# Kernel tuning notes

Hardware: AMD Instinct MI355X
Metric: run time of the kernel (lower is better)

The kernel has to match this reference:

```python
import jax, jax.numpy as jnp
import numpy as np

S0 = 192
C = [16, 32, 48, 64, 80]      # nPlanes = m*i, m=16, 5 strides
SL = [192, 96, 48, 24, 12]    # spatial size per level
OFF27 = jnp.asarray(np.stack(np.meshgrid(*([[-1, 0, 1]] * 3), indexing='ij'), -1).reshape(-1, 3), jnp.int32)
OFF8 = jnp.asarray(np.stack(np.meshgrid(*([[0, 1]] * 3), indexing='ij'), -1).reshape(-1, 3), jnp.int32)


def _flat(c, S):
    return (c[..., 0] * S + c[..., 1]) * S + c[..., 2]


def _grid(coords, S):
    g = jnp.full((S * S * S,), -1, jnp.int32)
    return g.at[_flat(coords, S)].set(jnp.arange(coords.shape[0], dtype=jnp.int32))


def _subconv(feat, coords, grid, S, W):
    # submanifold 3x3x3 conv over active sites only; W: [27, a, b]
    nb = coords[:, None, :] + OFF27                      # [N,27,3]
    valid = jnp.all((nb >= 0) & (nb < S), axis=-1)
    idx = grid[_flat(jnp.clip(nb, 0, S - 1), S)]         # [N,27]
    valid = valid & (idx >= 0)
    g = jnp.where(valid[..., None], feat[jnp.maximum(idx, 0)], 0.0)
    return jnp.einsum('nka,kab->nb', g, W)


def _downconv(feat, grid_f, S_f, out_coords, W):
    # kernel-2 stride-2 sparse conv; W: [8, a, b]
    src = out_coords[:, None, :] * 2 + OFF8              # [M,8,3]
    valid = jnp.all(src < S_f, axis=-1)
    idx = grid_f[_flat(src, S_f)]
    valid = valid & (idx >= 0)
    g = jnp.where(valid[..., None], feat[jnp.maximum(idx, 0)], 0.0)
    return jnp.einsum('nka,kab->nb', g, W)


def _bnrelu(x, g, b, eps=1e-4):
    # BatchNormLeakyReLU(leakiness=0) == BN (batch stats over active sites) + ReLU
    mu = jnp.mean(x, 0)
    var = jnp.mean((x - mu) ** 2, 0)
    return jax.nn.relu((x - mu) * jax.lax.rsqrt(var + eps) * g + b)


def _unpool(feat_c, grid_c, S_c, fine_coords, k):
    # UnPooling x k levels: copy coarse parent feature to each fine active site
    return feat_c[grid_c[_flat(fine_coords // (1 << k), S_c)]]


def _selection(scores):
    return (jax.nn.softmax(scores, axis=1)[:, 1:2] > 0.5).astype(scores.dtype)


def _forward(coords, features, w_in, blk_w, blk_g, blk_b, dn_g, dn_b, dn_w,
             ppn1_w, ppn1_sw, ppn2_w, ppn2_sw, ppn3_w, ppn3_pw, ppn3_sw):
    grids = [_grid(coords[l], SL[l]) for l in range(5)]
    x = _subconv(features, coords[0], grids[0], SL[0], w_in)   # input layer
    fmaps = [x]
    for i in range(4):  # encoder levels with residual blocks + downsample
        for r in range(2):
            h = _bnrelu(x, blk_g[i][2 * r], blk_b[i][2 * r])
            h = _subconv(h, coords[i], grids[i], SL[i], blk_w[i][2 * r])
            h = _bnrelu(h, blk_g[i][2 * r + 1], blk_b[i][2 * r + 1])
            h = _subconv(h, coords[i], grids[i], SL[i], blk_w[i][2 * r + 1])
            x = x + h  # ConcatTable(Identity, conv path) + AddTable, a==b
        x = _downconv(_bnrelu(x, dn_g[i], dn_b[i]), grids[i], SL[i], coords[i + 1], dn_w[i])
        fmaps.append(x)
    x = _subconv(x, coords[4], grids[4], SL[4], ppn1_w)
    ppn1_scores = x @ ppn1_sw                                   # 1x1 conv
    att1 = _unpool(_selection(ppn1_scores), grids[4], SL[4], coords[2], 2)
    y = fmaps[2] * att1                                         # Multiply at half_stride
    y = _subconv(y, coords[2], grids[2], SL[2], ppn2_w)
    ppn2_scores = y @ ppn2_sw
    att2 = _unpool(_selection(ppn2_scores), grids[2], SL[2], coords[0], 2)
    z = fmaps[0] * att2
    z = _subconv(z, coords[0], grids[0], SL[0], ppn3_w)
    out0 = jnp.concatenate([z @ ppn3_pw, z @ ppn3_sw], axis=1)
    out1 = jnp.concatenate([coords[4].astype(out0.dtype), ppn1_scores], axis=1)
    out2 = jnp.concatenate([coords[2].astype(out0.dtype), ppn2_scores], axis=1)
    return out0, out1, out2


def _make_coords():
    rng = np.random.RandomState(0)
    c0 = np.unique(rng.randint(0, S0, size=(100000, 3)), axis=0).astype(np.int32)
    cs = [c0]
    for _ in range(4):
        cs.append(np.unique(cs[-1] // 2, axis=0).astype(np.int32))
    return cs


def setup_inputs():
    key = jax.random.key(0)
    ks = iter(jax.random.split(key, 64))
    cs = _make_coords()
    inp = {f'coords{l}': jnp.asarray(cs[l]) for l in range(5)}
    N0 = cs[0].shape[0]
    inp['features'] = jax.random.normal(next(ks), (N0, 1), jnp.float32)

    def w(k, shape, fan):
        return jax.random.normal(k, shape, jnp.float32) * (fan ** -0.5)

    inp['w_in'] = w(next(ks), (27, 1, C[0]), 27)
    for i in range(4):
        inp[f'blk_w{i}'] = w(next(ks), (4, 27, C[i], C[i]), 27 * C[i])
        inp[f'blk_g{i}'] = jnp.ones((4, C[i]), jnp.float32)
        inp[f'blk_b{i}'] = jnp.zeros((4, C[i]), jnp.float32)
        inp[f'dn_g{i}'] = jnp.ones((C[i],), jnp.float32)
        inp[f'dn_b{i}'] = jnp.zeros((C[i],), jnp.float32)
        inp[f'dn_w{i}'] = w(next(ks), (8, C[i], C[i + 1]), 8 * C[i])
    inp['ppn1_w'] = w(next(ks), (27, C[4], C[4]), 27 * C[4])
    inp['ppn1_sw'] = w(next(ks), (C[4], 2), C[4])
    inp['ppn2_w'] = w(next(ks), (27, C[2], C[2]), 27 * C[2])
    inp['ppn2_sw'] = w(next(ks), (C[2], 2), C[2])
    inp['ppn3_w'] = w(next(ks), (27, C[0], C[0]), 27 * C[0])
    inp['ppn3_pw'] = w(next(ks), (C[0], 3), C[0])
    inp['ppn3_sw'] = w(next(ks), (C[0], 2), C[0])
    return inp


def reference(features, w_in,
              blk_w0, blk_g0, blk_b0, dn_g0, dn_b0, dn_w0,
              blk_w1, blk_g1, blk_b1, dn_g1, dn_b1, dn_w1,
              blk_w2, blk_g2, blk_b2, dn_g2, dn_b2, dn_w2,
              blk_w3, blk_g3, blk_b3, dn_g3, dn_b3, dn_w3,
              ppn1_w, ppn1_sw, ppn2_w, ppn2_sw, ppn3_w, ppn3_pw, ppn3_sw,
              coords0, coords1, coords2, coords3, coords4):
    coords = [coords0, coords1, coords2, coords3, coords4]
    return _forward(coords, features, w_in,
                    [blk_w0, blk_w1, blk_w2, blk_w3],
                    [blk_g0, blk_g1, blk_g2, blk_g3],
                    [blk_b0, blk_b1, blk_b2, blk_b3],
                    [dn_g0, dn_g1, dn_g2, dn_g3],
                    [dn_b0, dn_b1, dn_b2, dn_b3],
                    [dn_w0, dn_w1, dn_w2, dn_w3],
                    ppn1_w, ppn1_sw, ppn2_w, ppn2_sw, ppn3_w, ppn3_pw, ppn3_sw)
```

## Files before the change

kernel.cpp:

```cpp
#include <hip/hip_runtime.h>
#include <cstdint>
#include <cstddef>

#define TPB 256

typedef _Float16 f16x8 __attribute__((ext_vector_type(8)));
typedef float f32x4 __attribute__((ext_vector_type(4)));

__device__ __forceinline__ void block_sync_lds() {
    asm volatile("s_waitcnt lgkmcnt(0)" ::: "memory");
    __builtin_amdgcn_sched_barrier(0);
    __builtin_amdgcn_s_barrier();
    __builtin_amdgcn_sched_barrier(0);
}


static __global__ void kscatter(int* __restrict__ grid, const int* __restrict__ coords,
                                int N, int S) {
    int i = blockIdx.x * blockDim.x + threadIdx.x;
    if (i >= N) return;
    int x = coords[3 * i], y = coords[3 * i + 1], z = coords[3 * i + 2];
    grid[(x * S + y) * S + z] = i;
}

static __global__ void knbr27(int* __restrict__ nbr, const int* __restrict__ coords,
                              const int* __restrict__ grid, int N, int S, int zr) {
    int t = blockIdx.x * blockDim.x + threadIdx.x;
    if (t >= N * 27) return;
    int n = t / 27, k = t - 27 * n;
    int x = coords[3 * n]     + (k / 9) - 1;
    int y = coords[3 * n + 1] + ((k / 3) % 3) - 1;
    int z = coords[3 * n + 2] + (k % 3) - 1;
    int v = -1;
    if ((unsigned)x < (unsigned)S && (unsigned)y < (unsigned)S && (unsigned)z < (unsigned)S)
        v = grid[(x * S + y) * S + z];
    nbr[t] = (v < 0) ? zr : v;
}

static __global__ void kdown8(int* __restrict__ dn, const int* __restrict__ coords,
                              const int* __restrict__ grid, int M, int S_f, int zr) {
    int t = blockIdx.x * blockDim.x + threadIdx.x;
    if (t >= M * 8) return;
    int n = t >> 3, k = t & 7;
    int x = coords[3 * n] * 2     + ((k >> 2) & 1);
    int y = coords[3 * n + 1] * 2 + ((k >> 1) & 1);
    int z = coords[3 * n + 2] * 2 + (k & 1);
    int v = grid[(x * S_f + y) * S_f + z];
    dn[t] = (v < 0) ? zr : v;
}

static __global__ void kup(int* __restrict__ up, const int* __restrict__ cf,
                           const int* __restrict__ gc, int N, int Sc) {
    int n = blockIdx.x * blockDim.x + threadIdx.x;
    if (n >= N) return;
    int x = cf[3 * n] >> 2, y = cf[3 * n + 1] >> 2, z = cf[3 * n + 2] >> 2;
    up[n] = gc[(x * Sc + y) * Sc + z];
}

static __global__ void ksplitw(_Float16* __restrict__ dst, const float* __restrict__ src,
                               int KREAL, int KPAD, int A, int B) {
    int t = blockIdx.x * blockDim.x + threadIdx.x;
    if (t >= KPAD * A * B) return;
    int a = t % A;
    int b = (t / A) % B;
    int k = t / (A * B);
    float v = (k < KREAL) ? src[((size_t)k * A + a) * B + b] : 0.0f;
    _Float16 hi = (_Float16)v;
    _Float16 lo = (_Float16)(v - (float)hi);
    size_t row = ((size_t)k * B + b) * (size_t)(2 * A);
    dst[row + a] = hi;
    dst[row + A + a] = lo;
}


static __global__ void kstats(double* __restrict__ st, const float* __restrict__ x,
                              int N, int C) {
    extern __shared__ double sh[];
    int tid = threadIdx.x;
    int c = tid % C, rl = tid / C;
    double s = 0.0, q = 0.0;
    int base = blockIdx.x * 256 + rl * 64;
    for (int it = 0; it < 64; it++) {
        int r = base + it;
        if (r < N) {
            double v = (double)x[(size_t)r * C + c];
            s += v;
            q = fma(v, v, q);
        }
    }
    double* ss = sh;
    double* sq = sh + 4 * C;
    ss[tid] = s; sq[tid] = q;
    __syncthreads();
    if (tid < C) {
        double S = ss[tid] + ss[tid + C] + ss[tid + 2 * C] + ss[tid + 3 * C];
        double Q = sq[tid] + sq[tid + C] + sq[tid + 2 * C] + sq[tid + 3 * C];
        atomicAdd(&st[tid], S);
        atomicAdd(&st[80 + tid], Q);
    }
}

static __global__ void kbnrelu_h(_Float16* __restrict__ y, const float4* __restrict__ x,
                                 const double* __restrict__ st, const float* __restrict__ g,
                                 const float* __restrict__ b, int N, int C) {
    __shared__ float sc[80], bh[80];
    int tid = threadIdx.x;
    if (tid < C) {
        double invN = 1.0 / (double)N;
        double S = 0.0, Q = 0.0;
#pragma unroll
        for (int c = 0; c < 16; c++) {
            S += st[c * 160 + tid];
            Q += st[c * 160 + 80 + tid];
        }
        double mu = S * invN;
        double var = Q * invN - mu * mu;
        float s = g[tid] * rsqrtf((float)var + 1e-4f);
        sc[tid] = s;
        bh[tid] = b[tid] - (float)mu * s;
    }
    __syncthreads();
    int C8 = C >> 3;
    int chunks = (N + 1) * C8;
    int t = blockIdx.x * blockDim.x + tid;
    if (t >= chunks) return;
    int n = t / C8, cc = t - n * C8;
    f16x8 hi = {}, lo = {};
    if (n < N) {
        float4 q0 = x[n * (C >> 2) + cc * 2];
        float4 q1 = x[n * (C >> 2) + cc * 2 + 1];
        float v[8] = {q0.x, q0.y, q0.z, q0.w, q1.x, q1.y, q1.z, q1.w};
#pragma unroll
        for (int j = 0; j < 8; j++) {
            float r = fmaxf(fmaf(v[j], sc[cc * 8 + j], bh[cc * 8 + j]), 0.0f);
            _Float16 h = (_Float16)r;
            hi[j] = h;
            lo[j] = (_Float16)(r - (float)h);
        }
    }
    *(f16x8*)&y[(size_t)n * 2 * C + cc * 8] = hi;
    *(f16x8*)&y[(size_t)n * 2 * C + C + cc * 8] = lo;
}

static __global__ void kcvt_h(_Float16* __restrict__ y, const float4* __restrict__ x,
                              int N, int C) {
    int C8 = C >> 3;
    int t = blockIdx.x * blockDim.x + threadIdx.x;
    if (t >= (N + 1) * C8) return;
    int n = t / C8, cc = t - n * C8;
    f16x8 hi = {}, lo = {};
    if (n < N) {
        float4 q0 = x[n * (C >> 2) + cc * 2];
        float4 q1 = x[n * (C >> 2) + cc * 2 + 1];
        float v[8] = {q0.x, q0.y, q0.z, q0.w, q1.x, q1.y, q1.z, q1.w};
#pragma unroll
        for (int j = 0; j < 8; j++) {
            _Float16 h = (_Float16)v[j];
            hi[j] = h;
            lo[j] = (_Float16)(v[j] - (float)h);
        }
    }
    *(f16x8*)&y[(size_t)n * 2 * C + cc * 8] = hi;
    *(f16x8*)&y[(size_t)n * 2 * C + C + cc * 8] = lo;
}

static __global__ void kmulatt_h(_Float16* __restrict__ y, const float4* __restrict__ fmap,
                                 const int* __restrict__ up, const float* __restrict__ sc,
                                 int N, int C) {
    int C8 = C >> 3;
    int t = blockIdx.x * blockDim.x + threadIdx.x;
    if (t >= (N + 1) * C8) return;
    int n = t / C8, cc = t - n * C8;
    f16x8 hi = {}, lo = {};
    if (n < N) {
        int p = up[n];
        float att = (sc[2 * p + 1] > sc[2 * p]) ? 1.0f : 0.0f;
        float4 q0 = fmap[n * (C >> 2) + cc * 2];
        float4 q1 = fmap[n * (C >> 2) + cc * 2 + 1];
        float v[8] = {q0.x, q0.y, q0.z, q0.w, q1.x, q1.y, q1.z, q1.w};
#pragma unroll
        for (int j = 0; j < 8; j++) {
            float r = v[j] * att;
            _Float16 h = (_Float16)r;
            hi[j] = h;
            lo[j] = (_Float16)(r - (float)h);
        }
    }
    *(f16x8*)&y[(size_t)n * 2 * C + cc * 8] = hi;
    *(f16x8*)&y[(size_t)n * 2 * C + C + cc * 8] = lo;
}


template <int A, int B, int TAPS, int TPI, int TR, int MT, int KG, bool ADD>
__launch_bounds__(256, 2)
static __global__ void kconvmf(float* __restrict__ out, const _Float16* __restrict__ feat,
                               const int* __restrict__ nbr, const _Float16* __restrict__ Wsp,
                               const float* __restrict__ res, double* __restrict__ stp,
                               int N, int zr) {
    constexpr int NT_W = B / 16;
    static_assert(TR == 4 * MT * 16, "tile/wave mismatch");
    constexpr int KPT = (TPI == 1) ? ((A + 31) & ~31)
                      : (TPI == 2) ? ((A + 15) & ~15)
                                   : ((A + 7) & ~7);
    constexpr int KT = TPI * KPT;
    static_assert(KT % 32 == 0, "KT must be multiple of 32");
    constexpr int KSTEPS = KT / 32;
    constexpr int KTCH = KT / 8;
    constexpr int PKT = (KTCH == 12) ? 16 : KTCH;
    static_assert(PKT == 8 || PKT == 16, "bad PKT");
    constexpr int RH = PKT * 8;
    constexpr int QQ = KPT / 8;
    constexpr int AQ = A / 8;
    constexpr int A2 = 2 * A;
    constexpr int ITERS = (TAPS + TPI - 1) / TPI;
    constexpr int IPG = (ITERS + KG - 1) / KG;
    constexpr int WROWS = 2 * B;
    constexpr int WSBH = WROWS * RH;
    constexpr int WTOT = WROWS * KTCH;
    constexpr int WPT = (WTOT + 255) / 256;

    __shared__ __attribute__((aligned(16))) _Float16 wsb[2 * WSBH];
    __shared__ double sred[(KG == 1) ? 4 * 2 * B : 1];

    const int tid = threadIdx.x;

    int bx;
    {
        int nwg = gridDim.x, bid = blockIdx.x;
        int q = nwg >> 3, r = nwg & 7, xcd = bid & 7, ix = bid >> 3;
        bx = (xcd < r) ? xcd * (q + 1) + ix : r * (q + 1) + (xcd - r) * q + ix;
    }
    const int row0 = bx * TR;
    const int it0 = (KG > 1) ? blockIdx.y * IPG : 0;
    const int it1 = (KG > 1) ? ((it0 + IPG < ITERS) ? it0 + IPG : ITERS) : ITERS;

    const int lane = tid & 63, wid = tid >> 6;
    const int lrow = lane & 15, lgrp = lane >> 4;
    const int mb = wid * MT * 16;

    int w_lds[WPT], w_off[WPT];
    bool w_ok[WPT], w_real[WPT];
#pragma unroll
    for (int i = 0; i < WPT; i++) {
        int task = tid + i * 256;
        bool ok = (WTOT % 256 == 0) || (task < WTOT);
        int tc = ok ? task : 0;
        int q = tc % KTCH;
        int row = tc / KTCH;
        int bcol = row % B, pp = row / B;
        int t = q / QQ, qq = q - t * QQ;
        w_lds[i] = row * RH + (q ^ (row & (PKT - 1))) * 8;
        w_off[i] = (t * B + bcol) * A2 + pp * A + qq * 8;
        w_ok[i] = ok;
        w_real[i] = ok && (qq < AQ);
    }
    int rowm[MT];
#pragma unroll
    for (int mt = 0; mt < MT; mt++) rowm[mt] = row0 + mb + mt * 16 + lrow;

    f32x4 acc[MT][NT_W];
#pragma unroll
    for (int mt = 0; mt < MT; mt++)
#pragma unroll
        for (int nt = 0; nt < NT_W; nt++)
            acc[mt][nt] = (f32x4){0.f, 0.f, 0.f, 0.f};

    int nidA[MT][TPI], nidB[MT][TPI];
    f16x8 faA[MT][KSTEPS][2], faB[MT][KSTEPS][2];
    f16x8 wg[WPT];

    auto loadnbr = [&](auto& nd, int it) {
        int tb = it * TPI;
#pragma unroll
        for (int mt = 0; mt < MT; mt++)
#pragma unroll
            for (int t = 0; t < TPI; t++)
                nd[mt][t] = (rowm[mt] < N && tb + t < TAPS)
                          ? nbr[(size_t)rowm[mt] * TAPS + tb + t] : zr;
    };
    auto loadA = [&](auto& fd, const auto& nd) {
#pragma unroll
        for (int mt = 0; mt < MT; mt++)
#pragma unroll
            for (int ks = 0; ks < KSTEPS; ks++) {
                int qc = ks * 4 + lgrp;
                int t = qc / QQ;
                int cq = qc - t * QQ;
                int id;
                if constexpr (TPI == 1) id = nd[mt][0];
                else if constexpr (TPI == 2) id = (t == 0) ? nd[mt][0] : nd[mt][1];
                else {
                    int lo2 = (t == 0) ? nd[mt][0] : nd[mt][1];
                    int hi2 = (t == 2) ? nd[mt][2] : nd[mt][3];
                    id = (t < 2) ? lo2 : hi2;
                }
                const _Float16* p = feat + (size_t)id * A2 + cq * 8;
                if constexpr (QQ > AQ) {
                    bool okc = (cq < AQ);
                    fd[mt][ks][0] = okc ? *(const f16x8*)p : (f16x8){};
                    fd[mt][ks][1] = okc ? *(const f16x8*)(p + A) : (f16x8){};
                } else {
                    fd[mt][ks][0] = *(const f16x8*)p;
                    fd[mt][ks][1] = *(const f16x8*)(p + A);
                }
            }
    };
    auto loadW = [&](int it) {
        size_t base = (size_t)it * TPI * B * A2;
#pragma unroll
        for (int i = 0; i < WPT; i++)
            wg[i] = w_real[i] ? *(const f16x8*)&Wsp[base + w_off[i]] : (f16x8){};
    };
    auto storeW = [&](int c) {
        _Float16* d = wsb + c * WSBH;
#pragma unroll
        for (int i = 0; i < WPT; i++)
            if (w_ok[i]) *(f16x8*)&d[w_lds[i]] = wg[i];
    };
    auto domfma = [&](const auto& fd, int cb) {
#pragma unroll
        for (int ks = 0; ks < KSTEPS; ++ks) {
            const int qc = ks * 4 + lgrp;
            f16x8 bh[NT_W], bl[NT_W];
#pragma unroll
            for (int nt = 0; nt < NT_W; ++nt) {
                int rH = nt * 16 + lrow;
                bh[nt] = *(const f16x8*)&wsb[cb + rH * RH + (qc ^ (rH & (PKT - 1))) * 8];
                int rL = B + rH;
                bl[nt] = *(const f16x8*)&wsb[cb + rL * RH + (qc ^ (rL & (PKT - 1))) * 8];
            }
#pragma unroll
            for (int mt = 0; mt < MT; ++mt)
#pragma unroll
                for (int nt = 0; nt < NT_W; ++nt) {
                    acc[mt][nt] = __builtin_amdgcn_mfma_f32_16x16x32_f16(fd[mt][ks][0], bh[nt], acc[mt][nt], 0, 0, 0);
                    acc[mt][nt] = __builtin_amdgcn_mfma_f32_16x16x32_f16(fd[mt][ks][1], bh[nt], acc[mt][nt], 0, 0, 0);
                    acc[mt][nt] = __builtin_amdgcn_mfma_f32_16x16x32_f16(fd[mt][ks][0], bl[nt], acc[mt][nt], 0, 0, 0);
                }
        }
    };

    loadnbr(nidA, it0);
    loadA(faA, nidA);
    loadW(it0);
    storeW(0);
    if (it0 + 1 < it1) loadnbr(nidB, it0 + 1);
    block_sync_lds();
    if (it0 + 1 < it1) loadW(it0 + 1);

    int cur = 0;
    auto body = [&](const auto& fc, auto& fn, auto& nc, const auto& nn, int it) {
        const bool m1 = (it + 1 < it1), m2 = (it + 2 < it1);
        if (m1) {
            storeW(cur ^ 1);
            loadA(fn, nn);
        }
        if (m2) loadnbr(nc, it + 2);
        domfma(fc, cur * WSBH);
        if (m2) loadW(it + 2);
        if (m1) block_sync_lds();
        cur ^= 1;
    };
    for (int it = it0; it < it1; ) {
        body(faA, faB, nidA, nidB, it); ++it;
        if (it >= it1) break;
        body(faB, faA, nidB, nidA, it); ++it;
    }

    const bool dostats = (stp != nullptr);
    double ssum[NT_W], sqs[NT_W];
#pragma unroll
    for (int nt = 0; nt < NT_W; nt++) { ssum[nt] = 0.0; sqs[nt] = 0.0; }
#pragma unroll
    for (int mt = 0; mt < MT; ++mt) {
        int gr0 = row0 + mb + mt * 16 + lgrp * 4;
#pragma unroll
        for (int nt = 0; nt < NT_W; ++nt) {
            int gc = nt * 16 + lrow;
#pragma unroll
            for (int j = 0; j < 4; ++j) {
                int r = gr0 + j;
                if (r < N) {
                    size_t o = (size_t)r * B + gc;
                    if (KG > 1) {
                        atomicAdd(&out[o], acc[mt][nt][j]);
                    } else {
                        float v = acc[mt][nt][j];
                        if (ADD) v += res[o];
                        out[o] = v;
                        if (dostats) {
                            double dv = (double)v;
                            ssum[nt] += dv;
                            sqs[nt] = fma(dv, dv, sqs[nt]);
                        }
                    }
                }
            }
        }
    }
    if (KG == 1) {
        if (dostats) {
#pragma unroll
            for (int nt = 0; nt < NT_W; nt++) {
                ssum[nt] += __shfl_xor(ssum[nt], 16, 64);
                ssum[nt] += __shfl_xor(ssum[nt], 32, 64);
                sqs[nt] += __shfl_xor(sqs[nt], 16, 64);
                sqs[nt] += __shfl_xor(sqs[nt], 32, 64);
            }
            if (lgrp == 0) {
#pragma unroll
                for (int nt = 0; nt < NT_W; nt++) {
                    sred[(wid * 2 + 0) * B + nt * 16 + lrow] = ssum[nt];
                    sred[(wid * 2 + 1) * B + nt * 16 + lrow] = sqs[nt];
                }
            }
            __syncthreads();
            if (wid == 0) {
                double* sb = stp + (bx & 15) * 160;
                for (int c = lane; c < B; c += 64) {
                    double S = sred[c] + sred[2 * B + c] + sred[4 * B + c] + sred[6 * B + c];
                    double Q = sred[B + c] + sred[3 * B + c] + sred[5 * B + c] + sred[7 * B + c];
                    atomicAdd(&sb[c], S);
                    atomicAdd(&sb[80 + c], Q);
                }
            }
        }
    }
}

static __global__ void kconv_in(float* __restrict__ out, const float* __restrict__ f,
                                const int* __restrict__ nbr, const float* __restrict__ W,
                                int N, int zr) {
    int t = blockIdx.x * blockDim.x + threadIdx.x;
    if (t >= N * 4) return;
    int n = t >> 2, bq = t & 3;
    float4 acc = make_float4(0.f, 0.f, 0.f, 0.f);
    const float4* W4 = (const float4*)W;
    for (int k = 0; k < 27; k++) {
        int id = nbr[n * 27 + k];
        if (id == zr) continue;
        float v = f[id];
        float4 w = W4[k * 4 + bq];
        acc.x = fmaf(v, w.x, acc.x);
        acc.y = fmaf(v, w.y, acc.y);
        acc.z = fmaf(v, w.z, acc.z);
        acc.w = fmaf(v, w.w, acc.w);
    }
    ((float4*)out)[n * 4 + bq] = acc;
}


static __global__ void kscores(float* __restrict__ sc, const float* __restrict__ x,
                               const float* __restrict__ w, int N, int C) {
    int n = blockIdx.x * blockDim.x + threadIdx.x;
    if (n >= N) return;
    float s0 = 0.0f, s1 = 0.0f;
    const float* xr = x + (size_t)n * C;
    for (int c = 0; c < C; c++) {
        float v = xr[c];
        s0 = fmaf(v, w[2 * c], s0);
        s1 = fmaf(v, w[2 * c + 1], s1);
    }
    sc[2 * n] = s0;
    sc[2 * n + 1] = s1;
}

static __global__ void kout0(float* __restrict__ out, const float* __restrict__ z,
                             const float* __restrict__ pw, const float* __restrict__ sw,
                             int N) {
    int n = blockIdx.x * blockDim.x + threadIdx.x;
    if (n >= N) return;
    float o0 = 0, o1 = 0, o2 = 0, o3 = 0, o4 = 0;
    const float* zr = z + (size_t)n * 16;
#pragma unroll
    for (int c = 0; c < 16; c++) {
        float v = zr[c];
        o0 = fmaf(v, pw[3 * c], o0);
        o1 = fmaf(v, pw[3 * c + 1], o1);
        o2 = fmaf(v, pw[3 * c + 2], o2);
        o3 = fmaf(v, sw[2 * c], o3);
        o4 = fmaf(v, sw[2 * c + 1], o4);
    }
    float* r = out + (size_t)n * 5;
    r[0] = o0; r[1] = o1; r[2] = o2; r[3] = o3; r[4] = o4;
}

static __global__ void koutc(float* __restrict__ out, const int* __restrict__ coords,
                             const float* __restrict__ sc, int N) {
    int n = blockIdx.x * blockDim.x + threadIdx.x;
    if (n >= N) return;
    float* r = out + (size_t)n * 5;
    r[0] = (float)coords[3 * n];
    r[1] = (float)coords[3 * n + 1];
    r[2] = (float)coords[3 * n + 2];
    r[3] = sc[2 * n];
    r[4] = sc[2 * n + 1];
}


static inline int cdiv(long a, int b) { return (int)((a + b - 1) / b); }

static void conv(hipStream_t s, float* out, const _Float16* feat, const int* nbr,
                 const _Float16* Wsp, const float* res, double* stp,
                 int N, int A, int B, int TAPS, int zr) {
#define CASE(AA, BB, TT, TPI_, TR_, MT_, KG_)                                              \
    else if (A == AA && B == BB && TAPS == TT) {                                           \
        if (KG_ > 1 && !res) hipMemsetAsync(out, 0, (size_t)N * BB * 4, s);                \
        dim3 g(cdiv(N, TR_), KG_), blk(256);                                               \
        if (res) kconvmf<AA, BB, TT, TPI_, TR_, MT_, KG_, true><<<g, blk, 0, s>>>(out, feat, nbr, Wsp, res, stp, N, zr); \
        else     kconvmf<AA, BB, TT, TPI_, TR_, MT_, KG_, false><<<g, blk, 0, s>>>(out, feat, nbr, Wsp, nullptr, stp, N, zr); \
    }
    if (false) {}
    CASE(16, 16, 27,  4, 128,  2, 1)
    CASE(32, 32, 27,  2, 128,  2, 1)
    CASE(48, 48, 27,  2, 128,  2, 1)
    CASE(64, 64, 27,  1, 128,  2, 4)
    CASE(80, 80, 27,  1,  64,  1, 9)
    CASE(16, 32,  8,  4, 128,  2, 1)
    CASE(32, 48,  8,  2, 128,  2, 1)
    CASE(48, 64,  8,  2,  64,  1, 2)
    CASE(64, 80,  8,  1,  64,  1, 8)
#undef CASE
}

static void bnapply(hipStream_t s, _Float16* out, const float* x, double* st,
                    const float* g, const float* b, int N, int C, bool pre) {
    if (!pre)
        kstats<<<cdiv(N, 256), 4 * C, 8 * C * 2 * sizeof(double), s>>>(st, x, N, C);
    int chunks = (N + 1) * (C / 8);
    kbnrelu_h<<<cdiv(chunks, 256), 256, 0, s>>>(out, (const float4*)x, st, g, b, N, C);
}

extern "C" void kernel_launch(void* const* d_in, const int* in_sizes, int n_in,
                              void* d_out, int out_size, void* d_ws, size_t ws_size,
                              hipStream_t stream) {
    (void)n_in; (void)out_size; (void)ws_size;
    const int SL[5] = {192, 96, 48, 24, 12};
    const int C[5] = {16, 32, 48, 64, 80};
    int N[5];
    const int* coords[5];
    for (int l = 0; l < 5; l++) { N[l] = in_sizes[l] / 3; coords[l] = (const int*)d_in[l]; }
    const float* features = (const float*)d_in[5];
    const float* w_in = (const float*)d_in[6];
    const float *blk_w[4], *blk_g[4], *blk_b[4], *dn_g[4], *dn_b[4], *dn_w[4];
    for (int i = 0; i < 4; i++) {
        blk_w[i] = (const float*)d_in[7 + 6 * i];
        blk_g[i] = (const float*)d_in[8 + 6 * i];
        blk_b[i] = (const float*)d_in[9 + 6 * i];
        dn_g[i] = (const float*)d_in[10 + 6 * i];
        dn_b[i] = (const float*)d_in[11 + 6 * i];
        dn_w[i] = (const float*)d_in[12 + 6 * i];
    }
    const float* ppn1_w  = (const float*)d_in[31];
    const float* ppn1_sw = (const float*)d_in[32];
    const float* ppn2_w  = (const float*)d_in[33];
    const float* ppn2_sw = (const float*)d_in[34];
    const float* ppn3_w  = (const float*)d_in[35];
    const float* ppn3_pw = (const float*)d_in[36];
    const float* ppn3_sw = (const float*)d_in[37];
    float* dout = (float*)d_out;

    char* ws = (char*)d_ws;
    size_t off = 0;
    auto alloc = [&](size_t bytes) -> char* {
        off = (off + 255) & ~(size_t)255;
        char* p = ws + off;
        off += bytes;
        return p;
    };
    int* nbr[5];
    for (int l = 0; l < 5; l++) nbr[l] = (int*)alloc((size_t)N[l] * 27 * 4);
    int* down8[4];
    for (int i = 0; i < 4; i++) down8[i] = (int*)alloc((size_t)N[i + 1] * 8 * 4);
    int* up1 = (int*)alloc((size_t)N[2] * 4);
    int* up2 = (int*)alloc((size_t)N[0] * 4);
    double* stats = (double*)alloc((size_t)26 * 2560 * sizeof(double));
    _Float16* blkWsp[4];
    _Float16* dnWsp[4];
    for (int i = 0; i < 4; i++) {
        blkWsp[i] = (_Float16*)alloc((size_t)4 * 28 * C[i] * 2 * C[i] * 2);
        dnWsp[i] = (_Float16*)alloc((size_t)8 * C[i + 1] * 2 * C[i] * 2);
    }
    _Float16* p1Wsp = (_Float16*)alloc((size_t)27 * 80 * 160 * 2);
    _Float16* p2Wsp = (_Float16*)alloc((size_t)28 * 48 * 96 * 2);
    _Float16* p3Wsp = (_Float16*)alloc((size_t)28 * 16 * 32 * 2);
    float* fmap0 = (float*)alloc((size_t)N[0] * 16 * 4);
    float* fmap2 = (float*)alloc((size_t)N[2] * 48 * 4);
    float* sc1 = (float*)alloc((size_t)N[4] * 2 * 4);
    float* sc2 = (float*)alloc((size_t)N[2] * 2 * 4);

    size_t BIG = 0;
    for (int l = 0; l < 5; l++) {
        size_t s = (size_t)(N[l] + 1) * C[l] * 4;
        if (s > BIG) BIG = s;
    }
    BIG = (BIG + 255) & ~(size_t)255;
    off = (off + 255) & ~(size_t)255;
    size_t trans = off;
    int* grid[5];
    size_t gtot = 0;
    for (int l = 0; l < 5; l++) {
        grid[l] = (int*)(ws + trans + gtot);
        gtot += (size_t)SL[l] * SL[l] * SL[l] * 4;
    }
    float* B0 = (float*)(ws + trans);
    float* B1 = (float*)(ws + trans + BIG);
    float* B2 = (float*)(ws + trans + 2 * BIG);

    hipMemsetAsync(ws + trans, 0xFF, gtot, stream);
    hipMemsetAsync(stats, 0, (size_t)26 * 2560 * sizeof(double), stream);
    for (int l = 0; l < 5; l++)
        kscatter<<<cdiv(N[l], TPB), TPB, 0, stream>>>(grid[l], coords[l], N[l], SL[l]);
    for (int l = 0; l < 5; l++)
        knbr27<<<cdiv((long)N[l] * 27, TPB), TPB, 0, stream>>>(nbr[l], coords[l], grid[l], N[l], SL[l], N[l]);
    for (int i = 0; i < 4; i++)
        kdown8<<<cdiv((long)N[i + 1] * 8, TPB), TPB, 0, stream>>>(down8[i], coords[i + 1], grid[i], N[i + 1], SL[i], N[i]);
    kup<<<cdiv(N[2], TPB), TPB, 0, stream>>>(up1, coords[2], grid[4], N[2], 12);
    kup<<<cdiv(N[0], TPB), TPB, 0, stream>>>(up2, coords[0], grid[2], N[0], 48);
    for (int i = 0; i < 4; i++) {
        int Ci = C[i];
        for (int c = 0; c < 4; c++) {
            int n1 = 28 * Ci * Ci;
            ksplitw<<<cdiv(n1, TPB), TPB, 0, stream>>>(
                blkWsp[i] + (size_t)c * 28 * Ci * 2 * Ci,
                blk_w[i] + (size_t)c * 27 * Ci * Ci, 27, 28, Ci, Ci);
        }
        int n2 = 8 * Ci * C[i + 1];
        ksplitw<<<cdiv(n2, TPB), TPB, 0, stream>>>(dnWsp[i], dn_w[i], 8, 8, Ci, C[i + 1]);
    }
    ksplitw<<<cdiv(27 * 6400, TPB), TPB, 0, stream>>>(p1Wsp, ppn1_w, 27, 27, 80, 80);
    ksplitw<<<cdiv(28 * 2304, TPB), TPB, 0, stream>>>(p2Wsp, ppn2_w, 27, 28, 48, 48);
    ksplitw<<<cdiv(28 * 256, TPB), TPB, 0, stream>>>(p3Wsp, ppn3_w, 27, 28, 16, 16);

    int slot = 0;
    auto stn = [&]() { return stats + 2560 * (slot++); };
    auto stpeek = [&]() { return stats + 2560 * slot; };

    float* curX = B0;
    kconv_in<<<cdiv((long)N[0] * 4, TPB), TPB, 0, stream>>>(curX, features, nbr[0], w_in, N[0], N[0]);
    hipMemcpyAsync(fmap0, curX, (size_t)N[0] * 16 * 4, hipMemcpyDeviceToDevice, stream);

    auto others = [&](float* cur, float*& t1, float*& t2) {
        if (cur == B0) { t1 = B1; t2 = B2; }
        else if (cur == B1) { t1 = B0; t2 = B2; }
        else { t1 = B0; t2 = B1; }
    };

    bool entryPre = false;
    for (int i = 0; i < 4; i++) {
        int Ni = N[i], Ci = C[i];
        float *T1, *T2;
        others(curX, T1, T2);
        size_t wsl = (size_t)28 * Ci * 2 * Ci;
        bool fuseL = (i < 3);
        for (int r = 0; r < 2; r++) {
            bnapply(stream, (_Float16*)T1, curX, stn(), blk_g[i] + (2 * r) * Ci,
                    blk_b[i] + (2 * r) * Ci, Ni, Ci, r == 0 ? entryPre : fuseL);
            conv(stream, T2, (const _Float16*)T1, nbr[i], blkWsp[i] + (2 * r) * wsl,
                 nullptr, fuseL ? stpeek() : nullptr, Ni, Ci, Ci, 27, Ni);
            bnapply(stream, (_Float16*)T1, T2, stn(), blk_g[i] + (2 * r + 1) * Ci,
                    blk_b[i] + (2 * r + 1) * Ci, Ni, Ci, fuseL);
            conv(stream, curX, (const _Float16*)T1, nbr[i], blkWsp[i] + (2 * r + 1) * wsl,
                 curX, fuseL ? stpeek() : nullptr, Ni, Ci, Ci, 27, Ni);
        }
        bnapply(stream, (_Float16*)T1, curX, stn(), dn_g[i], dn_b[i], Ni, Ci, fuseL);
        bool fuseD = (i < 2);
        conv(stream, T2, (const _Float16*)T1, down8[i], dnWsp[i], nullptr,
             fuseD ? stpeek() : nullptr, N[i + 1], Ci, C[i + 1], 8, Ni);
        entryPre = fuseD;
        if (i == 1)
            hipMemcpyAsync(fmap2, T2, (size_t)N[2] * 48 * 4, hipMemcpyDeviceToDevice, stream);
        curX = T2;
    }

    float *T1, *T2;
    others(curX, T1, T2);
    kcvt_h<<<cdiv((N[4] + 1) * 10, TPB), TPB, 0, stream>>>((_Float16*)T1, (const float4*)curX, N[4], 80);
    conv(stream, T2, (const _Float16*)T1, nbr[4], p1Wsp, nullptr, nullptr, N[4], 80, 80, 27, N[4]);
    kscores<<<cdiv(N[4], TPB), TPB, 0, stream>>>(sc1, T2, ppn1_sw, N[4], 80);
    koutc<<<cdiv(N[4], TPB), TPB, 0, stream>>>(dout + (size_t)N[0] * 5, coords[4], sc1, N[4]);
    kmulatt_h<<<cdiv((long)(N[2] + 1) * 6, TPB), TPB, 0, stream>>>((_Float16*)curX, (const float4*)fmap2, up1, sc1, N[2], 48);
    conv(stream, T1, (const _Float16*)curX, nbr[2], p2Wsp, nullptr, nullptr, N[2], 48, 48, 27, N[2]);
    kscores<<<cdiv(N[2], TPB), TPB, 0, stream>>>(sc2, T1, ppn2_sw, N[2], 48);
    koutc<<<cdiv(N[2], TPB), TPB, 0, stream>>>(dout + (size_t)(N[0] + N[4]) * 5, coords[2], sc2, N[2]);
    kmulatt_h<<<cdiv((long)(N[0] + 1) * 2, TPB), TPB, 0, stream>>>((_Float16*)T2, (const float4*)fmap0, up2, sc2, N[0], 16);
    conv(stream, curX, (const _Float16*)T2, nbr[0], p3Wsp, nullptr, nullptr, N[0], 16, 16, 27, N[0]);
    kout0<<<cdiv(N[0], TPB), TPB, 0, stream>>>(dout, curX, ppn3_pw, ppn3_sw, N[0]);
}
```

Measured before the change: 1.288 ms.

## Stream gathered activations into LDS via direct global-to-LDS loads

Replaces the register double-buffer of gathered feature rows with global_load_lds transfers into a per-wave LDS staging area. Each iteration waits on vmcnt, copies the tile out of LDS into registers, then issues the next gather. The weight tile drops from double to single buffering, which adds a second barrier per iteration. The intent is to lower VGPR pressure and raise occupancy, at the cost of more LDS traffic and more synchronisation. Also changes the split-K factor for the 64->80 downconv and the thread count of one weight-split launch.

```diff
diff --git a/kernel.cpp b/kernel.cpp
--- a/kernel.cpp
+++ b/kernel.cpp
@@ -6,12 +6,19 @@
 
 typedef _Float16 f16x8 __attribute__((ext_vector_type(8)));
 typedef float f32x4 __attribute__((ext_vector_type(4)));
+typedef const __attribute__((address_space(1))) void* gp1_t;
+typedef __attribute__((address_space(3))) void* lp3_t;
 
 __device__ __forceinline__ void block_sync_lds() {
     asm volatile("s_waitcnt lgkmcnt(0)" ::: "memory");
     __builtin_amdgcn_sched_barrier(0);
     __builtin_amdgcn_s_barrier();
     __builtin_amdgcn_sched_barrier(0);
+}
+
+template <int N>
+__device__ __forceinline__ void waitcnt_vm() {
+    asm volatile("s_waitcnt vmcnt(%0)" :: "i"(N) : "memory");
 }
 
 
@@ -218,8 +225,11 @@
     constexpr int WSBH = WROWS * RH;
     constexpr int WTOT = WROWS * KTCH;
     constexpr int WPT = (WTOT + 255) / 256;
-
-    __shared__ __attribute__((aligned(16))) _Float16 wsb[2 * WSBH];
+    constexpr int SEGS = MT * KSTEPS * 2;
+    constexpr int NWAIT = MT * TPI + WPT;
+
+    __shared__ __attribute__((aligned(16))) _Float16 asb[4 * SEGS * 512];
+    __shared__ __attribute__((aligned(16))) _Float16 wsb[WSBH];
     __shared__ double sred[(KG == 1) ? 4 * 2 * B : 1];
 
     const int tid = threadIdx.x;
@@ -237,6 +247,7 @@
     const int lane = tid & 63, wid = tid >> 6;
     const int lrow = lane & 15, lgrp = lane >> 4;
     const int mb = wid * MT * 16;
+    const int awb = wid * SEGS * 512;
 
     int w_lds[WPT], w_off[WPT];
     bool w_ok[WPT], w_real[WPT];
@@ -266,7 +277,6 @@
             acc[mt][nt] = (f32x4){0.f, 0.f, 0.f, 0.f};
 
     int nidA[MT][TPI], nidB[MT][TPI];
-    f16x8 faA[MT][KSTEPS][2], faB[MT][KSTEPS][2];
     f16x8 wg[WPT];
 
     auto loadnbr = [&](auto& nd, int it) {
@@ -278,7 +288,7 @@
                 nd[mt][t] = (rowm[mt] < N && tb + t < TAPS)
                           ? nbr[(size_t)rowm[mt] * TAPS + tb + t] : zr;
     };
-    auto loadA = [&](auto& fd, const auto& nd) {
+    auto issueA = [&](const auto& nd) {
 #pragma unroll
         for (int mt = 0; mt < MT; mt++)
 #pragma unroll
@@ -294,15 +304,20 @@
                     int hi2 = (t == 2) ? nd[mt][2] : nd[mt][3];
                     id = (t < 2) ? lo2 : hi2;
                 }
-                const _Float16* p = feat + (size_t)id * A2 + cq * 8;
+                const _Float16* ph;
+                const _Float16* pl;
                 if constexpr (QQ > AQ) {
-                    bool okc = (cq < AQ);
-                    fd[mt][ks][0] = okc ? *(const f16x8*)p : (f16x8){};
-                    fd[mt][ks][1] = okc ? *(const f16x8*)(p + A) : (f16x8){};
+                    bool pad = (cq >= AQ);
+                    ph = pad ? (feat + (size_t)zr * A2)
+                             : (feat + (size_t)id * A2 + cq * 8);
+                    pl = pad ? ph : ph + A;
                 } else {
-                    fd[mt][ks][0] = *(const f16x8*)p;
-                    fd[mt][ks][1] = *(const f16x8*)(p + A);
+                    ph = feat + (size_t)id * A2 + cq * 8;
+                    pl = ph + A;
                 }
+                int sg = (mt * KSTEPS + ks) * 2;
+                __builtin_amdgcn_global_load_lds((gp1_t)ph, (lp3_t)&asb[awb + sg * 512], 16, 0, 0);
+                __builtin_amdgcn_global_load_lds((gp1_t)pl, (lp3_t)&asb[awb + (sg + 1) * 512], 16, 0, 0);
             }
     };
     auto loadW = [&](int it) {
@@ -311,13 +326,37 @@
         for (int i = 0; i < WPT; i++)
             wg[i] = w_real[i] ? *(const f16x8*)&Wsp[base + w_off[i]] : (f16x8){};
     };
-    auto storeW = [&](int c) {
-        _Float16* d = wsb + c * WSBH;
+    auto storeW = [&]() {
 #pragma unroll
         for (int i = 0; i < WPT; i++)
-            if (w_ok[i]) *(f16x8*)&d[w_lds[i]] = wg[i];
+            if (w_ok[i]) *(f16x8*)&wsb[w_lds[i]] = wg[i];
     };
-    auto domfma = [&](const auto& fd, int cb) {
+
+    loadnbr(nidA, it0);
+    issueA(nidA);
+    if (it0 + 1 < it1) loadnbr(nidB, it0 + 1);
+    loadW(it0);
+    storeW();
+    block_sync_lds();
+    if (it0 + 1 < it1) loadW(it0 + 1);
+
+    auto body = [&](auto& ncur, const auto& nnx, int it) {
+        const bool m1 = (it + 1 < it1), m2 = (it + 2 < it1);
+        if (m1) waitcnt_vm<NWAIT>(); else waitcnt_vm<0>();
+        __builtin_amdgcn_sched_barrier(0);
+        f16x8 fh[MT][KSTEPS], fl[MT][KSTEPS];
+#pragma unroll
+        for (int mt = 0; mt < MT; mt++)
+#pragma unroll
+            for (int ks = 0; ks < KSTEPS; ks++) {
+                int sg = (mt * KSTEPS + ks) * 2;
+                fh[mt][ks] = *(const f16x8*)&asb[awb + sg * 512 + lane * 8];
+                fl[mt][ks] = *(const f16x8*)&asb[awb + (sg + 1) * 512 + lane * 8];
+            }
+        asm volatile("s_waitcnt lgkmcnt(0)" ::: "memory");
+        __builtin_amdgcn_sched_barrier(0);
+        if (m1) issueA(nnx);
+        if (m2) loadnbr(ncur, it + 2);
 #pragma unroll
         for (int ks = 0; ks < KSTEPS; ++ks) {
             const int qc = ks * 4 + lgrp;
@@ -325,46 +364,30 @@
 #pragma unroll
             for (int nt = 0; nt < NT_W; ++nt) {
                 int rH = nt * 16 + lrow;
-                bh[nt] = *(const f16x8*)&wsb[cb + rH * RH + (qc ^ (rH & (PKT - 1))) * 8];
+                bh[nt] = *(const f16x8*)&wsb[rH * RH + (qc ^ (rH & (PKT - 1))) * 8];
                 int rL = B + rH;
-                bl[nt] = *(const f16x8*)&wsb[cb + rL * RH + (qc ^ (rL & (PKT - 1))) * 8];
+                bl[nt] = *(const f16x8*)&wsb[rL * RH + (qc ^ (rL & (PKT - 1))) * 8];
             }
 #pragma unroll
             for (int mt = 0; mt < MT; ++mt)
 #pragma unroll
                 for (int nt = 0; nt < NT_W; ++nt) {
-                    acc[mt][nt] = __builtin_amdgcn_mfma_f32_16x16x32_f16(fd[mt][ks][0], bh[nt], acc[mt][nt], 0, 0, 0);
-                    acc[mt][nt] = __builtin_amdgcn_mfma_f32_16x16x32_f16(fd[mt][ks][1], bh[nt], acc[mt][nt], 0, 0, 0);
-                    acc[mt][nt] = __builtin_amdgcn_mfma_f32_16x16x32_f16(fd[mt][ks][0], bl[nt], acc[mt][nt], 0, 0, 0);
+                    acc[mt][nt] = __builtin_amdgcn_mfma_f32_16x16x32_f16(fh[mt][ks], bh[nt], acc[mt][nt], 0, 0, 0);
+                    acc[mt][nt] = __builtin_amdgcn_mfma_f32_16x16x32_f16(fl[mt][ks], bh[nt], acc[mt][nt], 0, 0, 0);
+                    acc[mt][nt] = __builtin_amdgcn_mfma_f32_16x16x32_f16(fh[mt][ks], bl[nt], acc[mt][nt], 0, 0, 0);
                 }
         }
-    };
-
-    loadnbr(nidA, it0);
-    loadA(faA, nidA);
-    loadW(it0);
-    storeW(0);
-    if (it0 + 1 < it1) loadnbr(nidB, it0 + 1);
-    block_sync_lds();
-    if (it0 + 1 < it1) loadW(it0 + 1);
-
-    int cur = 0;
-    auto body = [&](const auto& fc, auto& fn, auto& nc, const auto& nn, int it) {
-        const bool m1 = (it + 1 < it1), m2 = (it + 2 < it1);
         if (m1) {
-            storeW(cur ^ 1);
-            loadA(fn, nn);
-        }
-        if (m2) loadnbr(nc, it + 2);
-        domfma(fc, cur * WSBH);
-        if (m2) loadW(it + 2);
-        if (m1) block_sync_lds();
-        cur ^= 1;
+            block_sync_lds();
+            storeW();
+            if (m2) loadW(it + 2);
+            block_sync_lds();
+        }
     };
     for (int it = it0; it < it1; ) {
-        body(faA, faB, nidA, nidB, it); ++it;
+        body(nidA, nidB, it); ++it;
         if (it >= it1) break;
-        body(faB, faA, nidB, nidA, it); ++it;
+        body(nidB, nidA, it); ++it;
     }
 
     const bool dostats = (stp != nullptr);
@@ -519,7 +542,7 @@
     CASE(16, 32,  8,  4, 128,  2, 1)
     CASE(32, 48,  8,  2, 128,  2, 1)
     CASE(48, 64,  8,  2,  64,  1, 2)
-    CASE(64, 80,  8,  1,  64,  1, 8)
+    CASE(64, 80,  8,  1,  64,  1, 2)
 #undef CASE
 }
 
@@ -628,7 +651,7 @@
         int n2 = 8 * Ci * C[i + 1];
         ksplitw<<<cdiv(n2, TPB), TPB, 0, stream>>>(dnWsp[i], dn_w[i], 8, 8, Ci, C[i + 1]);
     }
-    ksplitw<<<cdiv(27 * 6400, TPB), TPB, 0, stream>>>(p1Wsp, ppn1_w, 27, 27, 80, 80);
+    ksplitw<<<cdiv(28 * 6400, TPB), TPB, 0, stream>>>(p1Wsp, ppn1_w, 27, 27, 80, 80);
     ksplitw<<<cdiv(28 * 2304, TPB), TPB, 0, stream>>>(p2Wsp, ppn2_w, 27, 28, 48, 48);
     ksplitw<<<cdiv(28 * 256, TPB), TPB, 0, stream>>>(p3Wsp, ppn3_w, 27, 28, 16, 16);
 
```

Result: slower. 1.316 ms (+2.2%).
